# Performance work log

Measured on AMD Instinct MI355X. Metric: run time of the kernel, lower is better.

Reference implementation:

```python
import jax, jax.numpy as jnp
import numpy as np

EPS = 1e-12  # matches torch F.normalize eps
TEMPERATURE = 1.0


def _l2_normalize(x):
    n = jnp.sqrt(jnp.sum(x * x, axis=-1, keepdims=True))
    return x / jnp.maximum(n, EPS)


def setup_inputs() -> dict:
    key = jax.random.key(0)
    k1, k2 = jax.random.split(key)
    B, L, D, V = 2, 2048, 1024, 32000
    embeddings = jax.random.normal(k1, (B, L, D), dtype=jnp.float32)
    vocab_embeddings = jax.random.normal(k2, (V, D), dtype=jnp.float32)
    return {"embeddings": embeddings, "vocab_embeddings": vocab_embeddings, "k": 8}


def reference(embeddings, vocab_embeddings, k):
    """Soft KNN routing: cosine similarity -> top-k -> temperature softmax
    scattered into a full (B, L, V) probability distribution, plus hard
    argmax token ids (forward())."""
    B, L, D = embeddings.shape
    V = vocab_embeddings.shape[0]
    q = _l2_normalize(embeddings.reshape(-1, D))          # (N, D)
    vocab = _l2_normalize(vocab_embeddings)               # (V, D)
    sims = q @ vocab.T                                    # (N, V) cosine similarities
    topk_sim, topk_idx = jax.lax.top_k(sims, k)           # (N, k)
    probs_k = jax.nn.softmax(topk_sim / TEMPERATURE, axis=-1)
    N = q.shape[0]
    probs = jnp.zeros((N, V), dtype=probs_k.dtype)
    probs = probs.at[jnp.arange(N)[:, None], topk_idx].set(probs_k)
    probs = probs.reshape(B, L, V)                        # forward_soft output
    token_ids = topk_idx[:, 0].reshape(B, L)              # forward() hard routing (k=1)
    return probs, token_ids
```

## Files before the change

kernel.cpp:

```cpp
#include <hip/hip_runtime.h>
#include <math.h>

typedef unsigned int u32;
typedef unsigned char u8;
typedef long i64;
typedef float f32x16 __attribute__((ext_vector_type(16)));

static constexpr int N = 4096;
static constexpr int D = 1024;
static constexpr int V = 32000;
static constexpr int K = 8;
static constexpr int BM = 128;
static constexpr int BV = 256;
static constexpr int BK = 128;
static constexpr int NTILES = V / BV;
static constexpr int NG = 16;
static constexpr int NCAND = NG * K;
static constexpr int T24 = 24;
static constexpr int CPL = NCAND / 64;
static constexpr int GRID = (N / BM) * NG;
static constexpr u32 PSENT = 0x00800000u;

static constexpr size_t OUT_PROB_BYTES = (size_t)N * V * 4;
static constexpr size_t CAND_OFS = 83886080;
static constexpr size_t ZOFS = CAND_OFS + (size_t)N * NCAND * 4;
static constexpr size_t NZ4 = (OUT_PROB_BYTES - ZOFS) / 16;
static constexpr size_t NQZ4 = CAND_OFS / 16;

static_assert(N % BM == 0 && V % BV == 0, "tiling");
static_assert(ZOFS % 16 == 0, "align");
static_assert(NZ4 == (size_t)209 * GRID * 256, "zero quota exact");
static_assert(NQZ4 == (size_t)20 * (N / 4) * 256, "rescore zero quota exact");

__device__ __forceinline__ u8 f2fp8(float f) {
  u32 u = __float_as_uint(f);
  u32 sign = (u >> 24) & 0x80u;
  u32 au = u & 0x7FFFFFFFu;
  if (au < 0x3D800000u) {
    int m = (int)(__uint_as_float(au) * 512.0f + 0.5f);
    return (u8)(sign | (u32)m);
  }
  au += 0x7FFFFu + ((au >> 20) & 1u);
  if (au >= 0x43E00000u) return (u8)(sign | 0x7Eu);
  u32 e = (au >> 23) - 120u;
  return (u8)(sign | (e << 3) | ((au >> 20) & 7u));
}
__device__ __forceinline__ u32 flipbits(float v) {
  u32 u = __float_as_uint(v);
  return u ^ (((u32)((int)u >> 31)) | 0x80000000u);
}
__device__ __forceinline__ float unpackval(u32 p) {
  u32 s = p | 2047u;
  u32 u = (s & 0x80000000u) ? (s ^ 0x80000000u) : ~s;
  return __uint_as_float(u);
}
__device__ __forceinline__ void insert8(u32 pv[K], u32 x) {
  if (x <= pv[K - 1]) return;
  bool g[K];
#pragma unroll
  for (int j = 0; j < K; ++j) g[j] = x > pv[j];
#pragma unroll
  for (int j = K - 1; j >= 1; --j)
    pv[j] = g[j - 1] ? pv[j - 1] : (g[j] ? x : pv[j]);
  if (g[0]) pv[0] = x;
}

__global__ void zero_kernel(float4* __restrict__ p, int n4) {
  int i = blockIdx.x * blockDim.x + threadIdx.x;
  int stride = gridDim.x * blockDim.x;
  float4 z = make_float4(0.f, 0.f, 0.f, 0.f);
  for (; i < n4; i += stride) p[i] = z;
}

__global__ void normcvt_kernel(const float* __restrict__ x, float* __restrict__ inv,
                               u32* __restrict__ o) {
  int row = blockIdx.x;
  const float4* xr = reinterpret_cast<const float4*>(x + (size_t)row * D);
  float4 v = xr[threadIdx.x];
  float ss = v.x * v.x + v.y * v.y + v.z * v.z + v.w * v.w;
#pragma unroll
  for (int off = 32; off > 0; off >>= 1) ss += __shfl_down(ss, off, 64);
  __shared__ float wsum[4];
  if ((threadIdx.x & 63) == 0) wsum[threadIdx.x >> 6] = ss;
  __syncthreads();
  __shared__ float s_inv;
  if (threadIdx.x == 0) {
    float t = wsum[0] + wsum[1] + wsum[2] + wsum[3];
    float iv = 1.0f / fmaxf(sqrtf(t), 1e-12f);
    inv[row] = iv;
    s_inv = iv;
  }
  __syncthreads();
  float s = s_inv * 16.0f;
  u32 b0 = f2fp8(v.x * s), b1 = f2fp8(v.y * s), b2 = f2fp8(v.z * s), b3 = f2fp8(v.w * s);
  o[row * (D / 4) + threadIdx.x] = b0 | (b1 << 8) | (b2 << 16) | (b3 << 24);
}

__global__ __launch_bounds__(256, 2)
void simtopk_kernel(const u8* __restrict__ qn, const u8* __restrict__ vn,
                    u32* __restrict__ cand, float4* __restrict__ zout) {
  __shared__ __align__(16) u8 sh[(BV + BM) * BK];

  u8* v_sh = sh;
  u8* q_sh = sh + BV * BK;

  const int tid = threadIdx.x;
  const int bid = blockIdx.x;
  const int u_ = bid >> 3;
  const int rb = u_ & 31;
  const int grp = (bid & 7) * 2 + (u_ >> 5);
  const int t0 = (grp * NTILES) >> 4;
  const int t1 = ((grp + 1) * NTILES) >> 4;
  const int rbase = rb * BM;
  const int wid = tid >> 6, l = tid & 63;
  const int wv = wid >> 1, wq = wid & 1;
  const int h = l >> 5, lid = l & 31;
  const int srow = l >> 3;
  const int sk = ((l & 7) ^ srow) << 4;

  const float4 zf4 = make_float4(0.f, 0.f, 0.f, 0.f);

  u32 pv[2][K];
#pragma unroll
  for (int n = 0; n < 2; ++n)
#pragma unroll
    for (int j = 0; j < K; ++j) pv[n][j] = PSENT;
  float tminf[2] = {-3.0e38f, -3.0e38f};

  for (int ti = t0; ti < t1; ++ti) {
    const int cb = (ti - t0) * BV;
    f32x16 acc[4][2];
#pragma unroll
    for (int m = 0; m < 4; ++m)
#pragma unroll
      for (int n = 0; n < 2; ++n)
#pragma unroll
        for (int r = 0; r < 16; ++r) acc[m][n][r] = 0.f;

    for (int kk = 0; kk < D / BK; ++kk) {
      __syncthreads();
      {
        int it = (ti - t0) * 8 + kk;
#pragma unroll
        for (int j = 0; j < 4; ++j) {
          int s = it * 4 + j;
          if (s < 209) zout[(size_t)s * (GRID * 256) + bid * 256 + tid] = zf4;
        }
      }
      const int kb = kk * BK;
#pragma unroll
      for (int c = 0; c < 8; ++c) {
        int seg = c * 4 + wid;
        const u8* gs = vn + (size_t)(ti * BV + seg * 8 + srow) * D + kb + sk;
        __builtin_amdgcn_global_load_lds((const __attribute__((address_space(1))) void*)gs,
            (__attribute__((address_space(3))) void*)(v_sh + seg * 1024), 16, 0, 0);
      }
#pragma unroll
      for (int c = 0; c < 4; ++c) {
        int seg = c * 4 + wid;
        const u8* gs = qn + (size_t)(rbase + seg * 8 + srow) * D + kb + sk;
        __builtin_amdgcn_global_load_lds((const __attribute__((address_space(1))) void*)gs,
            (__attribute__((address_space(3))) void*)(q_sh + seg * 1024), 16, 0, 0);
      }
      __syncthreads();
      __builtin_amdgcn_s_setprio(1);
#pragma unroll
      for (int t = 0; t < 8; ++t) {
        i64 vf[4], qf[2];
#pragma unroll
        for (int m = 0; m < 4; ++m) {
          int row = wv * 128 + m * 32 + lid;
          int byte = row * BK + (((t ^ (row & 7)) << 4) | (h << 3));
          vf[m] = *reinterpret_cast<const i64*>(v_sh + byte);
        }
#pragma unroll
        for (int n = 0; n < 2; ++n) {
          int row = wq * 64 + n * 32 + lid;
          int byte = row * BK + (((t ^ (row & 7)) << 4) | (h << 3));
          qf[n] = *reinterpret_cast<const i64*>(q_sh + byte);
        }
#pragma unroll
        for (int m = 0; m < 4; ++m)
#pragma unroll
          for (int n = 0; n < 2; ++n)
            acc[m][n] = __builtin_amdgcn_mfma_f32_32x32x16_fp8_fp8(vf[m], qf[n], acc[m][n], 0, 0, 0);
      }
      __builtin_amdgcn_s_setprio(0);
    }

#pragma unroll
    for (int n = 0; n < 2; ++n) {
#pragma unroll
      for (int m = 0; m < 4; ++m) {
        f32x16 a = acc[m][n];
        float x01 = fmaxf(a[0], a[1]),   x23 = fmaxf(a[2], a[3]);
        float x45 = fmaxf(a[4], a[5]),   x67 = fmaxf(a[6], a[7]);
        float x89 = fmaxf(a[8], a[9]),   xab = fmaxf(a[10], a[11]);
        float xcd = fmaxf(a[12], a[13]), xef = fmaxf(a[14], a[15]);
        float mx = fmaxf(fmaxf(fmaxf(x01, x23), fmaxf(x45, x67)),
                         fmaxf(fmaxf(x89, xab), fmaxf(xcd, xef)));
        if (mx > tminf[n]) {
          const int cidb = cb + wv * 128 + m * 32 + 4 * h;
#pragma unroll
          for (int r = 0; r < 16; ++r) {
            float v = a[r];
            if (v > tminf[n]) {
              int cid = cidb + (r & 3) + 8 * (r >> 2);
              u32 p = (flipbits(v) & 0xFFFFF800u) | (u32)(2047 - cid);
              insert8(pv[n], p);
            }
          }
          tminf[n] = unpackval(pv[n][K - 1]);
        }
      }
    }
  }

  __syncthreads();
  u32* marr = (u32*)sh;
#pragma unroll
  for (int n = 0; n < 2; ++n)
#pragma unroll
    for (int j = 0; j < K; ++j)
      marr[((wq * 64 + n * 32 + lid) * 4 + (wv * 2 + h)) * K + j] = pv[n][j];
  __syncthreads();
  if (tid < BM) {
    u32 fv[K];
#pragma unroll
    for (int j = 0; j < K; ++j) fv[j] = PSENT;
#pragma unroll
    for (int c4 = 0; c4 < 4; ++c4)
#pragma unroll
      for (int j = 0; j < K; ++j) insert8(fv, marr[(tid * 4 + c4) * K + j]);
#pragma unroll
    for (int j = 0; j < K; ++j)
      cand[(size_t)(rbase + tid) * NCAND + grp * K + j] = fv[j];
  }
}

__global__ __launch_bounds__(256)
void rescore_kernel(const u32* __restrict__ cand,
                    const float* __restrict__ emb, const float* __restrict__ vocab,
                    const float* __restrict__ invq, const float* __restrict__ invv,
                    float* __restrict__ res_p, int* __restrict__ res_i,
                    float4* __restrict__ zq) {
  const int tid = threadIdx.x, wid = tid >> 6, l = tid & 63;
  const int row = blockIdx.x * 4 + wid;

  {
    const float4 zf4 = make_float4(0.f, 0.f, 0.f, 0.f);
    size_t base = (size_t)blockIdx.x * 256 + tid;
#pragma unroll
    for (int i = 0; i < 20; ++i)
      zq[(size_t)i * ((N / 4) * 256) + base] = zf4;
  }

  float4 q[4];
#pragma unroll
  for (int t = 0; t < 4; ++t)
    q[t] = *(reinterpret_cast<const float4*>(emb + (size_t)row * D) + t * 64 + l);
  float iqr = invq[row];

  u32 pl[CPL]; int li[CPL];
#pragma unroll
  for (int t = 0; t < CPL; ++t) {
    int e = l * CPL + t;
    u32 p = cand[(size_t)row * NCAND + e];
    int grp = e >> 3;
    int tile0 = (grp * NTILES) >> 4;
    pl[t] = p;
    li[t] = tile0 * BV + 2047 - (int)(p & 2047u);
  }

  int cidx[T24];
#pragma unroll
  for (int jr = 0; jr < T24; ++jr) {
    u32 bp = pl[0]; int bi = li[0];
#pragma unroll
    for (int t = 1; t < CPL; ++t)
      if (pl[t] > bp || (pl[t] == bp && li[t] < bi)) { bp = pl[t]; bi = li[t]; }
#pragma unroll
    for (int off = 32; off > 0; off >>= 1) {
      u32 op = (u32)__shfl_xor((int)bp, off, 64); int oi = __shfl_xor(bi, off, 64);
      if (op > bp || (op == bp && oi < bi)) { bp = op; bi = oi; }
    }
    cidx[jr] = bi;
#pragma unroll
    for (int t = 0; t < CPL; ++t) if (li[t] == bi) pl[t] = 0u;
  }

  float sv[T24];
#pragma unroll
  for (int jr = 0; jr < T24; ++jr) {
    int ix = cidx[jr];
    const float4* vr = reinterpret_cast<const float4*>(vocab + (size_t)ix * D);
    float s = 0.f;
#pragma unroll
    for (int t = 0; t < 4; ++t) {
      float4 vv = vr[t * 64 + l];
      s += q[t].x * vv.x + q[t].y * vv.y + q[t].z * vv.z + q[t].w * vv.w;
    }
#pragma unroll
    for (int off = 32; off > 0; off >>= 1) s += __shfl_xor(s, off, 64);
    sv[jr] = s * iqr * invv[ix];
  }

  float pvv[K]; int pii[K];
#pragma unroll
  for (int r8 = 0; r8 < K; ++r8) {
    float bv = sv[0]; int bi = cidx[0];
#pragma unroll
    for (int jr = 1; jr < T24; ++jr)
      if (sv[jr] > bv || (sv[jr] == bv && cidx[jr] < bi)) { bv = sv[jr]; bi = cidx[jr]; }
    pvv[r8] = bv; pii[r8] = bi;
#pragma unroll
    for (int jr = 0; jr < T24; ++jr) if (cidx[jr] == bi) sv[jr] = -3.0e38f;
  }

  float m = pvv[0], sum = 0.f, e8[K];
#pragma unroll
  for (int j = 0; j < K; ++j) { e8[j] = expf(pvv[j] - m); sum += e8[j]; }
  float isum = 1.f / sum;
  if (l == 0) {
#pragma unroll
    for (int j = 0; j < K; ++j) {
      res_p[row * K + j] = e8[j] * isum;
      res_i[row * K + j] = pii[j];
    }
  }
}

__global__ void scatter_kernel(const float* __restrict__ res_p, const int* __restrict__ res_i,
                               float* __restrict__ out) {
  int row = blockIdx.x * blockDim.x + threadIdx.x;
#pragma unroll
  for (int j = 0; j < K; ++j) out[(size_t)row * V + res_i[row * K + j]] = res_p[row * K + j];
  out[(size_t)N * V + row] = (float)res_i[row * K];
}

extern "C" void kernel_launch(void* const* d_in, const int* in_sizes, int n_in,
                              void* d_out, int out_size, void* d_ws, size_t ws_size,
                              hipStream_t stream) {
  const float* emb   = (const float*)d_in[0];
  const float* vocab = (const float*)d_in[1];
  float* out = (float*)d_out;

  u8* qn = (u8*)d_out;
  u8* vn = qn + (size_t)N * D;
  u32* cand = (u32*)((char*)d_out + CAND_OFS);
  float4* ztail = (float4*)((char*)d_out + ZOFS);

  float* wsf   = (float*)d_ws;
  float* invq  = wsf;
  float* invv  = wsf + N;
  float* res_p = wsf + N + V;
  int*   res_i = (int*)(wsf + N + V + N * K);

  normcvt_kernel<<<N, 256, 0, stream>>>(emb, invq, (u32*)qn);
  normcvt_kernel<<<V, 256, 0, stream>>>(vocab, invv, (u32*)vn);
  simtopk_kernel<<<GRID, 256, 0, stream>>>(qn, vn, cand, ztail);
  rescore_kernel<<<N / 4, 256, 0, stream>>>(cand, emb, vocab, invq, invv, res_p, res_i,
                                            (float4*)d_out);
  zero_kernel<<<192, 256, 0, stream>>>((float4*)((char*)d_out + CAND_OFS),
                                       (int)((ZOFS - CAND_OFS) / 16));
  scatter_kernel<<<N / 256, 256, 0, stream>>>(res_p, res_i, out);
}
```

Measured before the change: 458.5 us.

## Merge normalize launches, fold candidate zeroing into rescore, precompute LDS addresses

Combines the two normalize/convert launches into one kernel that uses one wavefront per row with four float4 loads, so there are fewer blocks and no shared-memory reduction. Removes the separate zero_kernel launch: each rescore block zeroes its own rows' candidate region after a barrier, once those candidates have been read into registers. In simtopk, global and LDS addresses and swizzle offsets are hoisted out of the inner loops and the tail-zeroing index is replaced by an incrementing pointer. The aim is to cut launch count and integer address arithmetic. The risk is that the in-kernel zeroing of candidates has to follow every read of them.

```diff
diff --git a/kernel.cpp b/kernel.cpp
--- a/kernel.cpp
+++ b/kernel.cpp
@@ -31,6 +31,7 @@
 static_assert(ZOFS % 16 == 0, "align");
 static_assert(NZ4 == (size_t)209 * GRID * 256, "zero quota exact");
 static_assert(NQZ4 == (size_t)20 * (N / 4) * 256, "rescore zero quota exact");
+static_assert((size_t)N * NCAND * 4 == (size_t)(N / 4) * 2048, "cand self-zero exact");
 
 __device__ __forceinline__ u8 f2fp8(float f) {
   u32 u = __float_as_uint(f);
@@ -65,44 +66,37 @@
   if (g[0]) pv[0] = x;
 }
 
-__global__ void zero_kernel(float4* __restrict__ p, int n4) {
-  int i = blockIdx.x * blockDim.x + threadIdx.x;
-  int stride = gridDim.x * blockDim.x;
-  float4 z = make_float4(0.f, 0.f, 0.f, 0.f);
-  for (; i < n4; i += stride) p[i] = z;
-}
-
-__global__ void normcvt_kernel(const float* __restrict__ x, float* __restrict__ inv,
-                               u32* __restrict__ o) {
-  int row = blockIdx.x;
-  const float4* xr = reinterpret_cast<const float4*>(x + (size_t)row * D);
-  float4 v = xr[threadIdx.x];
-  float ss = v.x * v.x + v.y * v.y + v.z * v.z + v.w * v.w;
-#pragma unroll
-  for (int off = 32; off > 0; off >>= 1) ss += __shfl_down(ss, off, 64);
-  __shared__ float wsum[4];
-  if ((threadIdx.x & 63) == 0) wsum[threadIdx.x >> 6] = ss;
-  __syncthreads();
-  __shared__ float s_inv;
-  if (threadIdx.x == 0) {
-    float t = wsum[0] + wsum[1] + wsum[2] + wsum[3];
-    float iv = 1.0f / fmaxf(sqrtf(t), 1e-12f);
-    inv[row] = iv;
-    s_inv = iv;
-  }
-  __syncthreads();
-  float s = s_inv * 16.0f;
-  u32 b0 = f2fp8(v.x * s), b1 = f2fp8(v.y * s), b2 = f2fp8(v.z * s), b3 = f2fp8(v.w * s);
-  o[row * (D / 4) + threadIdx.x] = b0 | (b1 << 8) | (b2 << 16) | (b3 << 24);
+__global__ __launch_bounds__(256)
+void normcvt_kernel(const float* __restrict__ emb, const float* __restrict__ vocab,
+                    float* __restrict__ inv, u32* __restrict__ o) {
+  const int gr = blockIdx.x * 4 + (threadIdx.x >> 6);
+  const int l = threadIdx.x & 63;
+  const float4* src = reinterpret_cast<const float4*>(
+      gr < N ? emb + (size_t)gr * D : vocab + (size_t)(gr - N) * D);
+  float4 v[4];
+  float ss = 0.f;
+#pragma unroll
+  for (int j = 0; j < 4; ++j) {
+    v[j] = src[j * 64 + l];
+    ss += v[j].x * v[j].x + v[j].y * v[j].y + v[j].z * v[j].z + v[j].w * v[j].w;
+  }
+#pragma unroll
+  for (int off = 32; off > 0; off >>= 1) ss += __shfl_xor(ss, off, 64);
+  float iv = 1.0f / fmaxf(sqrtf(ss), 1e-12f);
+  if (l == 0) inv[gr] = iv;
+  float s = iv * 16.0f;
+#pragma unroll
+  for (int j = 0; j < 4; ++j) {
+    u32 p = (u32)f2fp8(v[j].x * s) | ((u32)f2fp8(v[j].y * s) << 8) |
+            ((u32)f2fp8(v[j].z * s) << 16) | ((u32)f2fp8(v[j].w * s) << 24);
+    o[(size_t)gr * (D / 4) + j * 64 + l] = p;
+  }
 }
 
 __global__ __launch_bounds__(256, 2)
 void simtopk_kernel(const u8* __restrict__ qn, const u8* __restrict__ vn,
                     u32* __restrict__ cand, float4* __restrict__ zout) {
   __shared__ __align__(16) u8 sh[(BV + BM) * BK];
-
-  u8* v_sh = sh;
-  u8* q_sh = sh + BV * BK;
 
   const int tid = threadIdx.x;
   const int bid = blockIdx.x;
@@ -117,8 +111,20 @@
   const int h = l >> 5, lid = l & 31;
   const int srow = l >> 3;
   const int sk = ((l & 7) ^ srow) << 4;
+  const int csw = lid & 7;
+
+  u32 vbase[4], qbase[2];
+#pragma unroll
+  for (int m = 0; m < 4; ++m) vbase[m] = (u32)((wv * 128 + m * 32 + lid) * BK);
+#pragma unroll
+  for (int n = 0; n < 2; ++n) qbase[n] = (u32)(BV * BK + (wq * 64 + n * 32 + lid) * BK);
+  const u8* vsb = vn + (size_t)(wid * 8 + srow) * D + sk;
+  const u8* qsb = qn + (size_t)(rbase + wid * 8 + srow) * D + sk;
+  const u32 ldst = (u32)(wid * 1024);
 
   const float4 zf4 = make_float4(0.f, 0.f, 0.f, 0.f);
+  float4* zcur = zout + (size_t)bid * 256 + tid;
+  int zrem = 209;
 
   u32 pv[2][K];
 #pragma unroll
@@ -129,6 +135,7 @@
 
   for (int ti = t0; ti < t1; ++ti) {
     const int cb = (ti - t0) * BV;
+    const u8* vtile = vsb + (size_t)ti * BV * D;
     f32x16 acc[4][2];
 #pragma unroll
     for (int m = 0; m < 4; ++m)
@@ -139,46 +146,36 @@
 
     for (int kk = 0; kk < D / BK; ++kk) {
       __syncthreads();
-      {
-        int it = (ti - t0) * 8 + kk;
-#pragma unroll
-        for (int j = 0; j < 4; ++j) {
-          int s = it * 4 + j;
-          if (s < 209) zout[(size_t)s * (GRID * 256) + bid * 256 + tid] = zf4;
-        }
-      }
-      const int kb = kk * BK;
+#pragma unroll
+      for (int j = 0; j < 4; ++j) {
+        if (zrem > 0) { *zcur = zf4; zcur += GRID * 256; --zrem; }
+      }
+      const u8* vk = vtile + kk * BK;
+      const u8* qk = qsb + kk * BK;
 #pragma unroll
       for (int c = 0; c < 8; ++c) {
-        int seg = c * 4 + wid;
-        const u8* gs = vn + (size_t)(ti * BV + seg * 8 + srow) * D + kb + sk;
-        __builtin_amdgcn_global_load_lds((const __attribute__((address_space(1))) void*)gs,
-            (__attribute__((address_space(3))) void*)(v_sh + seg * 1024), 16, 0, 0);
+        __builtin_amdgcn_global_load_lds(
+            (const __attribute__((address_space(1))) void*)(vk + (size_t)c * 32 * D),
+            (__attribute__((address_space(3))) void*)(sh + ldst + c * 4096), 16, 0, 0);
       }
 #pragma unroll
       for (int c = 0; c < 4; ++c) {
-        int seg = c * 4 + wid;
-        const u8* gs = qn + (size_t)(rbase + seg * 8 + srow) * D + kb + sk;
-        __builtin_amdgcn_global_load_lds((const __attribute__((address_space(1))) void*)gs,
-            (__attribute__((address_space(3))) void*)(q_sh + seg * 1024), 16, 0, 0);
+        __builtin_amdgcn_global_load_lds(
+            (const __attribute__((address_space(1))) void*)(qk + (size_t)c * 32 * D),
+            (__attribute__((address_space(3))) void*)(sh + BV * BK + ldst + c * 4096), 16, 0, 0);
       }
       __syncthreads();
       __builtin_amdgcn_s_setprio(1);
 #pragma unroll
       for (int t = 0; t < 8; ++t) {
+        const u32 co = (u32)((((t ^ csw) << 4) | (h << 3)));
         i64 vf[4], qf[2];
 #pragma unroll
-        for (int m = 0; m < 4; ++m) {
-          int row = wv * 128 + m * 32 + lid;
-          int byte = row * BK + (((t ^ (row & 7)) << 4) | (h << 3));
-          vf[m] = *reinterpret_cast<const i64*>(v_sh + byte);
-        }
-#pragma unroll
-        for (int n = 0; n < 2; ++n) {
-          int row = wq * 64 + n * 32 + lid;
-          int byte = row * BK + (((t ^ (row & 7)) << 4) | (h << 3));
-          qf[n] = *reinterpret_cast<const i64*>(q_sh + byte);
-        }
+        for (int m = 0; m < 4; ++m)
+          vf[m] = *reinterpret_cast<const i64*>(sh + vbase[m] + co);
+#pragma unroll
+        for (int n = 0; n < 2; ++n)
+          qf[n] = *reinterpret_cast<const i64*>(sh + qbase[n] + co);
 #pragma unroll
         for (int m = 0; m < 4; ++m)
 #pragma unroll
@@ -243,12 +240,12 @@
                     const float* __restrict__ emb, const float* __restrict__ vocab,
                     const float* __restrict__ invq, const float* __restrict__ invv,
                     float* __restrict__ res_p, int* __restrict__ res_i,
-                    float4* __restrict__ zq) {
+                    float4* __restrict__ zq, float4* __restrict__ candz) {
   const int tid = threadIdx.x, wid = tid >> 6, l = tid & 63;
   const int row = blockIdx.x * 4 + wid;
+  const float4 zf4 = make_float4(0.f, 0.f, 0.f, 0.f);
 
   {
-    const float4 zf4 = make_float4(0.f, 0.f, 0.f, 0.f);
     size_t base = (size_t)blockIdx.x * 256 + tid;
 #pragma unroll
     for (int i = 0; i < 20; ++i)
@@ -271,6 +268,8 @@
     pl[t] = p;
     li[t] = tile0 * BV + 2047 - (int)(p & 2047u);
   }
+  __syncthreads();
+  if (tid < 128) candz[(size_t)blockIdx.x * 128 + tid] = zf4;
 
   int cidx[T24];
 #pragma unroll
@@ -356,12 +355,9 @@
   float* res_p = wsf + N + V;
   int*   res_i = (int*)(wsf + N + V + N * K);
 
-  normcvt_kernel<<<N, 256, 0, stream>>>(emb, invq, (u32*)qn);
-  normcvt_kernel<<<V, 256, 0, stream>>>(vocab, invv, (u32*)vn);
+  normcvt_kernel<<<(N + V) / 4, 256, 0, stream>>>(emb, vocab, invq, (u32*)qn);
   simtopk_kernel<<<GRID, 256, 0, stream>>>(qn, vn, cand, ztail);
   rescore_kernel<<<N / 4, 256, 0, stream>>>(cand, emb, vocab, invq, invv, res_p, res_i,
-                                            (float4*)d_out);
-  zero_kernel<<<192, 256, 0, stream>>>((float4*)((char*)d_out + CAND_OFS),
-                                       (int)((ZOFS - CAND_OFS) / 16));
+                                            (float4*)d_out, (float4*)cand);
   scatter_kernel<<<N / 256, 256, 0, stream>>>(res_p, res_i, out);
 }
```

After: 446.6 us (median of 3 runs). 1.03x faster.
